# Performance work log

Measured on AMD Instinct MI355X. Metric: run time of the kernel, lower is better.

Reference implementation:

```python
import jax, jax.numpy as jnp
import numpy as np

DIM = 1024
H = 16
DH = DIM // H
NF = 64
EPS = 1e-6


def setup_inputs() -> dict:
    key = jax.random.key(0)
    ks = jax.random.split(key, 10)
    B, L = 4, 4096
    s = 1.0 / np.sqrt(DIM)
    x = jax.random.normal(ks[0], (B, L, DIM), dtype=jnp.float32)
    Wq = jax.random.normal(ks[1], (DIM, DIM), dtype=jnp.float32) * s
    Wk = jax.random.normal(ks[2], (DIM, DIM), dtype=jnp.float32) * s
    Wv = jax.random.normal(ks[3], (DIM, DIM), dtype=jnp.float32) * s
    Wo = jax.random.normal(ks[4], (DIM, DIM), dtype=jnp.float32) * s
    bq = jax.random.normal(ks[5], (DIM,), dtype=jnp.float32) * s
    bk = jax.random.normal(ks[6], (DIM,), dtype=jnp.float32) * s
    bv = jax.random.normal(ks[7], (DIM,), dtype=jnp.float32) * s
    bo = jax.random.normal(ks[8], (DIM,), dtype=jnp.float32) * s
    # random-feature buffer: [num_repeats=1, H, DH, NF]; use repeat 0
    Wrf = jax.random.normal(ks[9], (1, H, DH, NF), dtype=jnp.float32)
    return {"x": x, "Wq": Wq, "bq": bq, "Wk": Wk, "bk": bk, "Wv": Wv,
            "bv": bv, "Wo": Wo, "bo": bo, "Wrf": Wrf}


def reference(x, Wq, bq, Wk, bk, Wv, bv, Wo, bo, Wrf):
    B, L, _ = x.shape
    W0 = Wrf[0]  # [H, DH, NF]

    def split_heads(y):
        return y.reshape(B, L, H, DH).transpose(0, 2, 1, 3)  # [B,H,L,DH]

    q = split_heads(x @ Wq.T + bq)
    k = split_heads(x @ Wk.T + bk)
    v = split_heads(x @ Wv.T + bv)

    # key summary: logits [B,H,L,NF], softmax over flattened (L*NF)
    logits = jnp.einsum('bhld,hdf->bhlf', k, W0) \
             - 0.5 * jnp.sum(k * k, axis=-1, keepdims=True)
    alpha = jax.nn.softmax(logits.reshape(B, H, L * NF), axis=2)
    alpha = alpha.reshape(B, H, L, NF)
    N = jnp.einsum('bhlf,bhld->bhfd', alpha, v)  # [B,H,NF,DH]
    D = jnp.sum(alpha, axis=2)                   # [B,H,NF]

    # query feature map: per-position softmax over features
    phi = jax.nn.softmax(jnp.einsum('bhld,hdf->bhlf', q, W0), axis=-1)

    num = jnp.einsum('bhlf,bhfd->bhld', phi, N)
    den = jnp.einsum('bhlf,bhf->bhl', phi, D)
    out = num / (den[..., None] + EPS)

    ctx = out.transpose(0, 2, 1, 3).reshape(B, L, DIM)
    return ctx @ Wo.T + bo
```

## Files before the change

kernel.cpp:

```cpp
#include <hip/hip_runtime.h>
#include <hip/hip_bf16.h>

constexpr int NB   = 4;
constexpr int SL   = 4096;
constexpr int DIMC = 1024;
constexpr int NH   = 16;
constexpr int DHC  = 64;
constexpr int NFC  = 64;
constexpr int NCHK = 8;
constexpr float FEPS = 1e-6f;

typedef __attribute__((ext_vector_type(8))) short bf16x8_t;
typedef __attribute__((ext_vector_type(4))) float f32x4_t;
typedef __attribute__((ext_vector_type(4))) short s16x4_t;

__device__ __forceinline__ void load_lds_16B(const short* g, short* l) {
  __builtin_amdgcn_global_load_lds(
      (__attribute__((address_space(1))) void*)(g),
      (__attribute__((address_space(3))) void*)(l), 16, 0, 0);
}

__global__ __launch_bounds__(256) void cast_f32_to_bf16(
    const float* __restrict__ in, short* __restrict__ out, int n)
{
  const int i = (blockIdx.x * 256 + threadIdx.x) * 4;
  if (i >= n) return;
  const f32x4_t v = *(const f32x4_t*)(in + i);
  s16x4_t o;
#pragma unroll
  for (int j = 0; j < 4; j++) {
    __hip_bfloat16 h = __float2bfloat16(v[j]);
    o[j] = *(short*)&h;
  }
  *(s16x4_t*)(out + i) = o;
}

__global__ __launch_bounds__(256) void prep_w0t_kernel(
    const float* __restrict__ Wrf, short* __restrict__ Whi, short* __restrict__ Wlo)
{
  const int h = blockIdx.x;
  for (int t = threadIdx.x; t < 4096; t += 256) {
    const int f = t >> 6, dh = t & 63;
    const float w = Wrf[(size_t)h * 4096 + dh * 64 + f];
    __hip_bfloat16 hi = __float2bfloat16(w);
    const float rem = w - __bfloat162float(hi);
    __hip_bfloat16 lo = __float2bfloat16(rem);
    Whi[(size_t)h * 4096 + t] = *(short*)&hi;
    Wlo[(size_t)h * 4096 + t] = *(short*)&lo;
  }
}

__global__ __launch_bounds__(256) void fuse_w0_kernel(
    const float* __restrict__ Wq, const float* __restrict__ bq,
    const float* __restrict__ Wrf,
    short* __restrict__ Wfh, short* __restrict__ Wfl, float* __restrict__ bqf)
{
  const int h = blockIdx.x, cb = blockIdx.y;
  __shared__ float sWq[64][64];
  __shared__ float sW0[64][64];
  for (int idx = threadIdx.x; idx < 4096; idx += 256) {
    const int d = idx >> 6, e = idx & 63;
    sWq[d][e] = Wq[(size_t)(h * 64 + d) * 1024 + cb * 64 + e];
    sW0[d][e] = Wrf[(size_t)h * 4096 + d * 64 + e];
  }
  __syncthreads();
  for (int idx = threadIdx.x; idx < 4096; idx += 256) {
    const int f = idx >> 6, cc = idx & 63;
    float acc = 0.f;
#pragma unroll
    for (int d = 0; d < 64; d++) acc = fmaf(sWq[d][cc], sW0[d][f], acc);
    const __hip_bfloat16 hi = __float2bfloat16(acc);
    const float rem = acc - __bfloat162float(hi);
    const __hip_bfloat16 lo = __float2bfloat16(rem);
    Wfh[(size_t)(h * 64 + f) * 1024 + cb * 64 + cc] = *(const short*)&hi;
    Wfl[(size_t)(h * 64 + f) * 1024 + cb * 64 + cc] = *(const short*)&lo;
  }
  if (cb == 0 && threadIdx.x < 64) {
    const int f = threadIdx.x;
    float acc = 0.f;
#pragma unroll
    for (int d = 0; d < 64; d++) acc = fmaf(bq[h * 64 + d], sW0[d][f], acc);
    bqf[h * 64 + f] = acc;
  }
}

template <int MODE>
__global__ __launch_bounds__(256) void gemm_lds_kernel(
    const short* __restrict__ A, const short* __restrict__ W,
    const float* __restrict__ bias, void* __restrict__ C0,
    void* __restrict__ C1, float* __restrict__ Ks)
{
  constexpr int K = 1024, N = 1024;
  const int lane = threadIdx.x & 63;
  const int wid  = threadIdx.x >> 6;
  const int sub  = lane & 15;
  const int quad = lane >> 4;
  const int wr   = (wid >> 1) * 64;
  const int wc   = (wid & 1) * 64;
  const int row0 = blockIdx.x * 128;
  const int col0 = blockIdx.y * 128;

  __shared__ short As[128 * 64];
  __shared__ short Bs[128 * 64];

  f32x4_t acc[4][4] = {};

  const int srow = lane >> 3;
  for (int k0 = 0; k0 < K; k0 += 64) {
#pragma unroll
    for (int t = 0; t < 4; t++) {
      const int R   = wid * 32 + t * 8;
      const int row = R + srow;
      const int c   = (lane & 7) ^ (row & 7);
      load_lds_16B(A + (size_t)(row0 + row) * K + k0 + c * 8, As + R * 64);
      load_lds_16B(W + (size_t)(col0 + row) * K + k0 + c * 8, Bs + R * 64);
    }
    __syncthreads();

    bf16x8_t a[2][4], b[2][4];
#pragma unroll
    for (int ks = 0; ks < 2; ks++) {
#pragma unroll
      for (int i = 0; i < 4; i++) {
        const int ra = wr + i * 16 + sub;
        a[ks][i] = *(const bf16x8_t*)(As + ra * 64 + (((ks * 4 + quad) ^ (ra & 7)) * 8));
        const int rb = wc + i * 16 + sub;
        b[ks][i] = *(const bf16x8_t*)(Bs + rb * 64 + (((ks * 4 + quad) ^ (rb & 7)) * 8));
      }
    }
#pragma unroll
    for (int ks = 0; ks < 2; ks++)
#pragma unroll
      for (int i = 0; i < 4; i++)
#pragma unroll
        for (int j = 0; j < 4; j++) {
          if constexpr (MODE == 5)
            acc[i][j] = __builtin_amdgcn_mfma_f32_16x16x32_bf16(b[ks][j], a[ks][i], acc[i][j], 0, 0, 0);
          else
            acc[i][j] = __builtin_amdgcn_mfma_f32_16x16x32_bf16(a[ks][i], b[ks][j], acc[i][j], 0, 0, 0);
        }
    __syncthreads();
  }

  const int rb0 = row0 + wr;
  const int cb0 = col0 + wc;
  if constexpr (MODE == 3) {
    __hip_bfloat16* chi = (__hip_bfloat16*)C0;
    __hip_bfloat16* clo = (__hip_bfloat16*)C1;
    float s[4][4];
#pragma unroll
    for (int i = 0; i < 4; i++)
#pragma unroll
      for (int r = 0; r < 4; r++) s[i][r] = 0.f;
#pragma unroll
    for (int j = 0; j < 4; j++) {
      const int col = cb0 + j * 16 + sub;
      const float bv = bias[col];
#pragma unroll
      for (int i = 0; i < 4; i++) {
        const int row = rb0 + i * 16 + quad * 4;
#pragma unroll
        for (int r = 0; r < 4; r++) {
          const float val = acc[i][j][r] + bv;
          const __hip_bfloat16 hi = __float2bfloat16(val);
          const float rem = val - __bfloat162float(hi);
          chi[(size_t)(row + r) * N + col] = hi;
          clo[(size_t)(row + r) * N + col] = __float2bfloat16(rem);
          s[i][r] = fmaf(val, val, s[i][r]);
        }
      }
    }
    {
      const int head = cb0 >> 6;
#pragma unroll
      for (int o = 1; o < 16; o <<= 1)
#pragma unroll
        for (int i = 0; i < 4; i++)
#pragma unroll
          for (int r = 0; r < 4; r++) s[i][r] += __shfl_xor(s[i][r], o);
      if (sub == 0) {
#pragma unroll
        for (int i = 0; i < 4; i++)
#pragma unroll
          for (int r = 0; r < 4; r++)
            Ks[(size_t)(rb0 + i * 16 + quad * 4 + r) * NH + head] = s[i][r];
      }
    }
  } else if constexpr (MODE == 5) {
    __hip_bfloat16* vT = (__hip_bfloat16*)C0;
    const int bb    = row0 >> 12;
    const int lbase = rb0 - (bb << 12);
#pragma unroll
    for (int j = 0; j < 4; j++) {
#pragma unroll
      for (int r = 0; r < 4; r++) {
        const int col = cb0 + j * 16 + quad * 4 + r;
        const int h = col >> 6, d = col & 63;
        const float bv = bias[col];
        const size_t rowbase = ((size_t)((bb * NH + h) * 64 + d)) * (size_t)SL;
#pragma unroll
        for (int i = 0; i < 4; i++) {
          const int l = lbase + i * 16 + sub;
          const int pos = (l & ~127) | (((((l >> 3) & 15) ^ (d & 15)) << 3) | (l & 7));
          vT[rowbase + pos] = __float2bfloat16(acc[i][j][r] + bv);
        }
      }
    }
  } else {
#pragma unroll
    for (int j = 0; j < 4; j++) {
      const int col = cb0 + j * 16 + sub;
      const float bv = bias[col];
#pragma unroll
      for (int i = 0; i < 4; i++) {
        const int row = rb0 + i * 16 + quad * 4;
#pragma unroll
        for (int r = 0; r < 4; r++) {
          const float val = acc[i][j][r] + bv;
          ((float*)C0)[(size_t)(row + r) * N + col] = val;
        }
      }
    }
  }
}

__global__ __launch_bounds__(256) void gemm_phi_kernel(
    const short* __restrict__ A, const short* __restrict__ Wh,
    const short* __restrict__ Wl, const float* __restrict__ bqf,
    const float* __restrict__ Df, short* __restrict__ ehi,
    short* __restrict__ elo, float* __restrict__ sbuf)
{
  constexpr int K = 1024;
  const int lane = threadIdx.x & 63;
  const int wid  = threadIdx.x >> 6;
  const int sub  = lane & 15;
  const int quad = lane >> 4;
  const int wr   = (wid >> 1) * 64;
  const int wc   = (wid & 1) * 64;
  const int row0 = blockIdx.x * 128;
  const int col0 = blockIdx.y * 128;

  __shared__ short As[128 * 64];
  __shared__ short Bhs[128 * 64];
  __shared__ short Bls[128 * 64];

  f32x4_t acc[4][4] = {};

  const int srow = lane >> 3;
  for (int k0 = 0; k0 < K; k0 += 64) {
#pragma unroll
    for (int t = 0; t < 4; t++) {
      const int R   = wid * 32 + t * 8;
      const int row = R + srow;
      const int c   = (lane & 7) ^ (row & 7);
      load_lds_16B(A  + (size_t)(row0 + row) * K + k0 + c * 8, As  + R * 64);
      load_lds_16B(Wh + (size_t)(col0 + row) * K + k0 + c * 8, Bhs + R * 64);
      load_lds_16B(Wl + (size_t)(col0 + row) * K + k0 + c * 8, Bls + R * 64);
    }
    __syncthreads();

#pragma unroll
    for (int ks = 0; ks < 2; ks++) {
      bf16x8_t a[4], bh[4], bl[4];
#pragma unroll
      for (int i = 0; i < 4; i++) {
        const int ra = wr + i * 16 + sub;
        a[i] = *(const bf16x8_t*)(As + ra * 64 + (((ks * 4 + quad) ^ (ra & 7)) * 8));
        const int rb = wc + i * 16 + sub;
        bh[i] = *(const bf16x8_t*)(Bhs + rb * 64 + (((ks * 4 + quad) ^ (rb & 7)) * 8));
        bl[i] = *(const bf16x8_t*)(Bls + rb * 64 + (((ks * 4 + quad) ^ (rb & 7)) * 8));
      }
#pragma unroll
      for (int i = 0; i < 4; i++)
#pragma unroll
        for (int j = 0; j < 4; j++) {
          acc[i][j] = __builtin_amdgcn_mfma_f32_16x16x32_bf16(a[i], bh[j], acc[i][j], 0, 0, 0);
          acc[i][j] = __builtin_amdgcn_mfma_f32_16x16x32_bf16(a[i], bl[j], acc[i][j], 0, 0, 0);
        }
      __syncthreads();
    }
  }

  const int rb0 = row0 + wr;
  const int cb0 = col0 + wc;
  const int b   = row0 >> 12;
  const int h   = cb0 >> 6;
  float bv[4], Dl[4];
#pragma unroll
  for (int j = 0; j < 4; j++) {
    const int f = j * 16 + sub;
    bv[j] = bqf[h * 64 + f];
    Dl[j] = Df[(b * NH + h) * 64 + f];
  }
#pragma unroll
  for (int i = 0; i < 4; i++) {
#pragma unroll
    for (int r = 0; r < 4; r++) {
      float v[4];
#pragma unroll
      for (int j = 0; j < 4; j++) v[j] = acc[i][j][r] + bv[j];
      float mx = fmaxf(fmaxf(v[0], v[1]), fmaxf(v[2], v[3]));
#pragma unroll
      for (int o = 1; o < 16; o <<= 1) mx = fmaxf(mx, __shfl_xor(mx, o));
      float e[4], se = 0.f, dt = 0.f;
#pragma unroll
      for (int j = 0; j < 4; j++) {
        e[j] = __expf(v[j] - mx);
        se += e[j];
        dt = fmaf(e[j], Dl[j], dt);
      }
#pragma unroll
      for (int o = 1; o < 16; o <<= 1) { se += __shfl_xor(se, o); dt += __shfl_xor(dt, o); }

      const int row = rb0 + i * 16 + quad * 4 + r;
      const size_t base = (size_t)row * DIMC + h * 64;
#pragma unroll
      for (int j = 0; j < 4; j++) {
        const __hip_bfloat16 hi = __float2bfloat16(e[j]);
        const float rem = e[j] - __bfloat162float(hi);
        const __hip_bfloat16 lo = __float2bfloat16(rem);
        ehi[base + j * 16 + sub] = *(const short*)&hi;
        elo[base + j * 16 + sub] = *(const short*)&lo;
      }
      if (sub == 0) sbuf[row * NH + h] = 1.f / (dt + FEPS * se);
    }
  }
}

__global__ __launch_bounds__(256) void feat_gemm_kernel(
    const short* __restrict__ xhi, const short* __restrict__ xlo,
    const short* __restrict__ Whi, const short* __restrict__ Wlo,
    float* __restrict__ outlog)
{
  const int lane = threadIdx.x & 63, wid = threadIdx.x >> 6;
  const int sub = lane & 15, quad = lane >> 4;
  const int h = blockIdx.y;
  const int tok0 = blockIdx.x * 128 + wid * 32;
  const short* Bh = Whi + (size_t)h * 4096;
  const short* Bl = Wlo + (size_t)h * 4096;

  f32x4_t acc[2][4] = {};
#pragma unroll
  for (int ks = 0; ks < 2; ks++) {
    const int ko = ks * 32 + quad * 8;
    bf16x8_t ah[2], al[2], bh[4], bl[4];
#pragma unroll
    for (int i = 0; i < 2; i++) {
      const size_t base = (size_t)(tok0 + i * 16 + sub) * DIMC + h * 64 + ko;
      ah[i] = *(const bf16x8_t*)(xhi + base);
      al[i] = *(const bf16x8_t*)(xlo + base);
    }
#pragma unroll
    for (int j = 0; j < 4; j++) {
      const size_t base = (size_t)(j * 16 + sub) * 64 + ko;
      bh[j] = *(const bf16x8_t*)(Bh + base);
      bl[j] = *(const bf16x8_t*)(Bl + base);
    }
#pragma unroll
    for (int i = 0; i < 2; i++)
#pragma unroll
      for (int j = 0; j < 4; j++) {
        acc[i][j] = __builtin_amdgcn_mfma_f32_16x16x32_bf16(ah[i], bh[j], acc[i][j], 0, 0, 0);
        acc[i][j] = __builtin_amdgcn_mfma_f32_16x16x32_bf16(al[i], bh[j], acc[i][j], 0, 0, 0);
        acc[i][j] = __builtin_amdgcn_mfma_f32_16x16x32_bf16(ah[i], bl[j], acc[i][j], 0, 0, 0);
      }
  }
#pragma unroll
  for (int i = 0; i < 2; i++)
#pragma unroll
    for (int j = 0; j < 4; j++)
#pragma unroll
      for (int r = 0; r < 4; r++)
        outlog[(size_t)(tok0 + i * 16 + quad * 4 + r) * DIMC + h * 64 + j * 16 + sub] = acc[i][j][r];
}

__global__ __launch_bounds__(256) void kv_summary_mfma(
    const float* __restrict__ klog, const float* __restrict__ ksq,
    const short* __restrict__ vT, float* __restrict__ pN, float* __restrict__ pD)
{
  const int chunk = blockIdx.x, h = blockIdx.y, b = blockIdx.z;
  const int tid  = threadIdx.x;
  const int lane = tid & 63, wid = tid >> 6;
  const int sub  = lane & 15, quad = lane >> 4;

  __shared__ short vTs[64 * 128];
  __shared__ short wTh[64 * 128];
  __shared__ short wTl[64 * 128];

  f32x4_t accN[4] = {};
  f32x4_t accD = {};
  bf16x8_t bones;
#pragma unroll
  for (int e = 0; e < 8; e++) bones[e] = (sub == 0) ? (short)0x3F80 : (short)0;

  const int tw_t  = tid >> 1;
  const int tw_f0 = (tid & 1) * 32;

  const size_t vbase = ((size_t)((b * NH + h) * 64)) * (size_t)SL;
  const int fbase = (wid * 16 + sub) * 128;

  for (int it = 0; it < 4; ++it) {
    const int l0 = chunk * 512 + it * 128;

#pragma unroll
    for (int q = 0; q < 4; q++) {
      const int dbase = wid * 16 + q * 4;
      const int d = dbase + (lane >> 4);
      load_lds_16B(vT + vbase + (size_t)d * SL + l0 + (lane & 15) * 8,
                   vTs + dbase * 128);
    }

    {
      const int tok = b * SL + l0 + tw_t;
      const float kq = 0.5f * ksq[tok * NH + h];
      const float* kr = klog + (size_t)tok * DIMC + h * 64 + tw_f0;
      f32x4_t kl[8];
#pragma unroll
      for (int v4 = 0; v4 < 8; v4++) kl[v4] = *(const f32x4_t*)(kr + v4 * 4);
#pragma unroll
      for (int v4 = 0; v4 < 8; v4++) {
#pragma unroll
        for (int e = 0; e < 4; e++) {
          const int f = tw_f0 + v4 * 4 + e;
          const float wv = __expf(kl[v4][e] - kq);
          const __hip_bfloat16 hi = __float2bfloat16(wv);
          const float rem = wv - __bfloat162float(hi);
          const __hip_bfloat16 lo = __float2bfloat16(rem);
          const int p = f * 128 + (((((tw_t >> 3) & 15) ^ (f & 15)) << 3) | (tw_t & 7));
          wTh[p] = *(const short*)&hi;
          wTl[p] = *(const short*)&lo;
        }
      }
    }
    __syncthreads();

#pragma unroll
    for (int ks = 0; ks < 4; ks++) {
      const int ch = ks * 4 + quad;
      const bf16x8_t ah = *(const bf16x8_t*)(wTh + fbase + ((ch ^ sub) << 3));
      const bf16x8_t al = *(const bf16x8_t*)(wTl + fbase + ((ch ^ sub) << 3));
      accD = __builtin_amdgcn_mfma_f32_16x16x32_bf16(ah, bones, accD, 0, 0, 0);
      accD = __builtin_amdgcn_mfma_f32_16x16x32_bf16(al, bones, accD, 0, 0, 0);
#pragma unroll
      for (int j = 0; j < 4; j++) {
        const bf16x8_t bv = *(const bf16x8_t*)(vTs + (j * 16 + sub) * 128 + ((ch ^ sub) << 3));
        accN[j] = __builtin_amdgcn_mfma_f32_16x16x32_bf16(ah, bv, accN[j], 0, 0, 0);
        accN[j] = __builtin_amdgcn_mfma_f32_16x16x32_bf16(al, bv, accN[j], 0, 0, 0);
      }
    }
    __syncthreads();
  }

  const size_t pbase = (size_t)((b * NH + h) * NCHK + chunk);
#pragma unroll
  for (int j = 0; j < 4; j++)
#pragma unroll
    for (int r = 0; r < 4; r++)
      pN[pbase * 4096 + (wid * 16 + quad * 4 + r) * 64 + j * 16 + sub] = accN[j][r];
  if (sub == 0) {
#pragma unroll
    for (int r = 0; r < 4; r++)
      pD[pbase * 64 + wid * 16 + quad * 4 + r] = accD[r];
  }
}

__global__ __launch_bounds__(256) void combine_nd_kernel(
    const float* __restrict__ pN, const float* __restrict__ pD,
    short* __restrict__ NfTh, short* __restrict__ NfTl, float* __restrict__ Df)
{
  const int bh = blockIdx.x, seg = blockIdx.y;
  __shared__ float sInv;
  float dsum = 0.f;
  if (threadIdx.x < 64) {
    for (int c = 0; c < NCHK; c++)
      dsum += pD[(size_t)(bh * NCHK + c) * 64 + threadIdx.x];
    float s = dsum;
#pragma unroll
    for (int o = 32; o; o >>= 1) s += __shfl_xor(s, o);
    if (threadIdx.x == 0) sInv = 1.f / s;
  }
  __syncthreads();
  const float inv = sInv;
  if (seg == 0 && threadIdx.x < 64) Df[bh * 64 + threadIdx.x] = dsum * inv;
  const int t = seg * 256 + threadIdx.x;
  float acc = 0.f;
  for (int c = 0; c < NCHK; c++)
    acc += pN[((size_t)(bh * NCHK + c)) * 4096 + t];
  const float val = acc * inv;
  const int f = t >> 6, d = t & 63;
  const __hip_bfloat16 hi = __float2bfloat16(val);
  const float rem = val - __bfloat162float(hi);
  const __hip_bfloat16 lo = __float2bfloat16(rem);
  NfTh[(size_t)bh * 4096 + d * 64 + f] = *(const short*)&hi;
  NfTl[(size_t)bh * 4096 + d * 64 + f] = *(const short*)&lo;
}

__global__ __launch_bounds__(256) void ctx_gemm_kernel(
    const short* __restrict__ ehi, const short* __restrict__ elo,
    const short* __restrict__ NfTh, const short* __restrict__ NfTl,
    const float* __restrict__ sbuf, __hip_bfloat16* __restrict__ ctx)
{
  const int lane = threadIdx.x & 63, wid = threadIdx.x >> 6;
  const int sub = lane & 15, quad = lane >> 4;
  const int h = blockIdx.y;
  const int tok0 = blockIdx.x * 128 + wid * 32;
  const int b = blockIdx.x >> 5;
  const short* Bh = NfTh + ((size_t)(b * NH + h)) * 4096;
  const short* Bl = NfTl + ((size_t)(b * NH + h)) * 4096;

  f32x4_t acc[2][4] = {};
#pragma unroll
  for (int ks = 0; ks < 2; ks++) {
    const int ko = ks * 32 + quad * 8;
    bf16x8_t ah[2], al[2], bh[4], bl[4];
#pragma unroll
    for (int i = 0; i < 2; i++) {
      const size_t base = (size_t)(tok0 + i * 16 + sub) * DIMC + h * 64 + ko;
      ah[i] = *(const bf16x8_t*)(ehi + base);
      al[i] = *(const bf16x8_t*)(elo + base);
    }
#pragma unroll
    for (int j = 0; j < 4; j++) {
      const size_t base = (size_t)(j * 16 + sub) * 64 + ko;
      bh[j] = *(const bf16x8_t*)(Bh + base);
      bl[j] = *(const bf16x8_t*)(Bl + base);
    }
#pragma unroll
    for (int i = 0; i < 2; i++)
#pragma unroll
      for (int j = 0; j < 4; j++) {
        acc[i][j] = __builtin_amdgcn_mfma_f32_16x16x32_bf16(ah[i], bh[j], acc[i][j], 0, 0, 0);
        acc[i][j] = __builtin_amdgcn_mfma_f32_16x16x32_bf16(al[i], bh[j], acc[i][j], 0, 0, 0);
        acc[i][j] = __builtin_amdgcn_mfma_f32_16x16x32_bf16(ah[i], bl[j], acc[i][j], 0, 0, 0);
      }
  }
#pragma unroll
  for (int i = 0; i < 2; i++)
#pragma unroll
    for (int r = 0; r < 4; r++) {
      const int token = tok0 + i * 16 + quad * 4 + r;
      const float sv = sbuf[token * NH + h];
#pragma unroll
      for (int j = 0; j < 4; j++)
        ctx[(size_t)token * DIMC + h * 64 + j * 16 + sub] =
            __float2bfloat16(acc[i][j][r] * sv);
    }
}

extern "C" void kernel_launch(void* const* d_in, const int* in_sizes, int n_in,
                              void* d_out, int out_size, void* d_ws, size_t ws_size,
                              hipStream_t stream) {
  (void)in_sizes; (void)n_in; (void)out_size; (void)ws_size;
  const float* x   = (const float*)d_in[0];
  const float* Wq  = (const float*)d_in[1];
  const float* bq  = (const float*)d_in[2];
  const float* Wk  = (const float*)d_in[3];
  const float* bk  = (const float*)d_in[4];
  const float* Wv  = (const float*)d_in[5];
  const float* bv  = (const float*)d_in[6];
  const float* Wo  = (const float*)d_in[7];
  const float* bo  = (const float*)d_in[8];
  const float* Wrf = (const float*)d_in[9];
  float* out = (float*)d_out;

  constexpr size_t MiB = 1u << 20;
  constexpr size_t KiB = 1u << 10;
  constexpr size_t NTOK = (size_t)NB * SL;
  constexpr size_t XN   = NTOK * DIMC;
  constexpr size_t WN   = (size_t)DIMC * DIMC;

  char* ws = (char*)d_ws;
  short* xb   = (short*)(ws);
  short* Wkb  = (short*)(ws + 32 * MiB);
  short* Wvb  = (short*)(ws + 34 * MiB);
  short* Wob  = (short*)(ws + 36 * MiB);
  short* W0Th = (short*)(ws + 40 * MiB);
  short* W0Tl = (short*)(ws + 40 * MiB + 128 * KiB);
  float* bqf  = (float*)(ws + 40 * MiB + 256 * KiB);
  float* ksq  = (float*)(ws + 41 * MiB);
  float* sbuf = (float*)(ws + 42 * MiB);
  float* pD   = (float*)(ws + 43 * MiB);
  short* NfTh = (short*)(ws + 43 * MiB + 512 * KiB);
  short* NfTl = (short*)(ws + 44 * MiB);
  float* Df   = (float*)(ws + 44 * MiB + 512 * KiB);
  float* klog = (float*)(ws + 45 * MiB);
  __hip_bfloat16* khi = (__hip_bfloat16*)(ws + 109 * MiB);
  __hip_bfloat16* klo = (__hip_bfloat16*)(ws + 141 * MiB);
  short* vTb  = (short*)(ws + 173 * MiB);
  float* pN   = (float*)(ws + 109 * MiB);
  short* Wqfh = (short*)(ws + 173 * MiB);
  short* Wqfl = (short*)(ws + 175 * MiB);
  short* ehi  = (short*)(ws + 45 * MiB);
  short* elo  = (short*)(ws + 77 * MiB);
  __hip_bfloat16* ctxb = (__hip_bfloat16*)xb;

  const dim3 blk(256);

  cast_f32_to_bf16<<<dim3(XN / 1024), blk, 0, stream>>>(x, xb, (int)XN);
  cast_f32_to_bf16<<<dim3(WN / 1024), blk, 0, stream>>>(Wk, Wkb, (int)WN);
  cast_f32_to_bf16<<<dim3(WN / 1024), blk, 0, stream>>>(Wv, Wvb, (int)WN);
  cast_f32_to_bf16<<<dim3(WN / 1024), blk, 0, stream>>>(Wo, Wob, (int)WN);
  prep_w0t_kernel<<<dim3(NH), blk, 0, stream>>>(Wrf, W0Th, W0Tl);

  const dim3 gg(NTOK / 128, DIMC / 128);
  gemm_lds_kernel<3><<<gg, blk, 0, stream>>>(xb, Wkb, bk, khi, klo, ksq);
  gemm_lds_kernel<5><<<gg, blk, 0, stream>>>(xb, Wvb, bv, vTb, nullptr, nullptr);

  feat_gemm_kernel<<<dim3(NTOK / 128, NH), blk, 0, stream>>>(
      (const short*)khi, (const short*)klo, W0Th, W0Tl, klog);

  kv_summary_mfma<<<dim3(NCHK, NH, NB), blk, 0, stream>>>(klog, ksq, vTb, pN, pD);
  fuse_w0_kernel<<<dim3(NH, 16), blk, 0, stream>>>(Wq, bq, Wrf, Wqfh, Wqfl, bqf);
  combine_nd_kernel<<<dim3(NB * NH, 16), blk, 0, stream>>>(pN, pD, NfTh, NfTl, Df);

  gemm_phi_kernel<<<gg, blk, 0, stream>>>(xb, Wqfh, Wqfl, bqf, Df, ehi, elo, sbuf);
  ctx_gemm_kernel<<<dim3(NTOK / 128, NH), blk, 0, stream>>>(
      ehi, elo, NfTh, NfTl, sbuf, ctxb);

  gemm_lds_kernel<0><<<gg, blk, 0, stream>>>((const short*)ctxb, Wob, bo, out, nullptr, nullptr);
}
```

Baseline: 491.1 us.

## Fuse key feature GEMM into KV summary kernel, dropping fp32 logit buffer

The separate feat_gemm kernel that wrote fp32 key logits (64 MiB) to global memory is removed. The kv summary kernel now loads the hi/lo bf16 key tiles and W0 into LDS, computes the logits with MFMA in-block, applies the exp, and reuses the LDS buffers for the transposed weights. This removes a large global write and read plus one launch. The cost is the logit GEMM running inside a small grid of 512 blocks, with an extra barrier and more LDS per block.

```diff
diff --git a/kernel.cpp b/kernel.cpp
--- a/kernel.cpp
+++ b/kernel.cpp
@@ -327,56 +327,11 @@
   }
 }
 
-__global__ __launch_bounds__(256) void feat_gemm_kernel(
-    const short* __restrict__ xhi, const short* __restrict__ xlo,
-    const short* __restrict__ Whi, const short* __restrict__ Wlo,
-    float* __restrict__ outlog)
-{
-  const int lane = threadIdx.x & 63, wid = threadIdx.x >> 6;
-  const int sub = lane & 15, quad = lane >> 4;
-  const int h = blockIdx.y;
-  const int tok0 = blockIdx.x * 128 + wid * 32;
-  const short* Bh = Whi + (size_t)h * 4096;
-  const short* Bl = Wlo + (size_t)h * 4096;
-
-  f32x4_t acc[2][4] = {};
-#pragma unroll
-  for (int ks = 0; ks < 2; ks++) {
-    const int ko = ks * 32 + quad * 8;
-    bf16x8_t ah[2], al[2], bh[4], bl[4];
-#pragma unroll
-    for (int i = 0; i < 2; i++) {
-      const size_t base = (size_t)(tok0 + i * 16 + sub) * DIMC + h * 64 + ko;
-      ah[i] = *(const bf16x8_t*)(xhi + base);
-      al[i] = *(const bf16x8_t*)(xlo + base);
-    }
-#pragma unroll
-    for (int j = 0; j < 4; j++) {
-      const size_t base = (size_t)(j * 16 + sub) * 64 + ko;
-      bh[j] = *(const bf16x8_t*)(Bh + base);
-      bl[j] = *(const bf16x8_t*)(Bl + base);
-    }
-#pragma unroll
-    for (int i = 0; i < 2; i++)
-#pragma unroll
-      for (int j = 0; j < 4; j++) {
-        acc[i][j] = __builtin_amdgcn_mfma_f32_16x16x32_bf16(ah[i], bh[j], acc[i][j], 0, 0, 0);
-        acc[i][j] = __builtin_amdgcn_mfma_f32_16x16x32_bf16(al[i], bh[j], acc[i][j], 0, 0, 0);
-        acc[i][j] = __builtin_amdgcn_mfma_f32_16x16x32_bf16(ah[i], bl[j], acc[i][j], 0, 0, 0);
-      }
-  }
-#pragma unroll
-  for (int i = 0; i < 2; i++)
-#pragma unroll
-    for (int j = 0; j < 4; j++)
-#pragma unroll
-      for (int r = 0; r < 4; r++)
-        outlog[(size_t)(tok0 + i * 16 + quad * 4 + r) * DIMC + h * 64 + j * 16 + sub] = acc[i][j][r];
-}
-
-__global__ __launch_bounds__(256) void kv_summary_mfma(
-    const float* __restrict__ klog, const float* __restrict__ ksq,
-    const short* __restrict__ vT, float* __restrict__ pN, float* __restrict__ pD)
+__global__ __launch_bounds__(256) void kv_fused_kernel(
+    const short* __restrict__ khi, const short* __restrict__ klo,
+    const short* __restrict__ W0h, const short* __restrict__ W0l,
+    const float* __restrict__ ksq, const short* __restrict__ vT,
+    float* __restrict__ pN, float* __restrict__ pD)
 {
   const int chunk = blockIdx.x, h = blockIdx.y, b = blockIdx.z;
   const int tid  = threadIdx.x;
@@ -384,8 +339,10 @@
   const int sub  = lane & 15, quad = lane >> 4;
 
   __shared__ short vTs[64 * 128];
-  __shared__ short wTh[64 * 128];
-  __shared__ short wTl[64 * 128];
+  __shared__ short w0hs[64 * 64];
+  __shared__ short w0ls[64 * 64];
+  __shared__ short uh[128 * 64];
+  __shared__ short ul[128 * 64];
 
   f32x4_t accN[4] = {};
   f32x4_t accD = {};
@@ -393,8 +350,14 @@
 #pragma unroll
   for (int e = 0; e < 8; e++) bones[e] = (sub == 0) ? (short)0x3F80 : (short)0;
 
-  const int tw_t  = tid >> 1;
-  const int tw_f0 = (tid & 1) * 32;
+#pragma unroll
+  for (int t = 0; t < 2; t++) {
+    const int R   = wid * 16 + t * 8;
+    const int row = R + (lane >> 3);
+    const int c   = (lane & 7) ^ (row & 7);
+    load_lds_16B(W0h + (size_t)h * 4096 + row * 64 + c * 8, w0hs + R * 64);
+    load_lds_16B(W0l + (size_t)h * 4096 + row * 64 + c * 8, w0ls + R * 64);
+  }
 
   const size_t vbase = ((size_t)((b * NH + h) * 64)) * (size_t)SL;
   const int fbase = (wid * 16 + sub) * 128;
@@ -409,26 +372,62 @@
       load_lds_16B(vT + vbase + (size_t)d * SL + l0 + (lane & 15) * 8,
                    vTs + dbase * 128);
     }
-
-    {
-      const int tok = b * SL + l0 + tw_t;
-      const float kq = 0.5f * ksq[tok * NH + h];
-      const float* kr = klog + (size_t)tok * DIMC + h * 64 + tw_f0;
-      f32x4_t kl[8];
-#pragma unroll
-      for (int v4 = 0; v4 < 8; v4++) kl[v4] = *(const f32x4_t*)(kr + v4 * 4);
-#pragma unroll
-      for (int v4 = 0; v4 < 8; v4++) {
-#pragma unroll
-        for (int e = 0; e < 4; e++) {
-          const int f = tw_f0 + v4 * 4 + e;
-          const float wv = __expf(kl[v4][e] - kq);
+#pragma unroll
+    for (int t = 0; t < 4; t++) {
+      const int R   = wid * 32 + t * 8;
+      const int row = R + (lane >> 3);
+      const int c   = (lane & 7) ^ (row & 7);
+      const size_t src = (size_t)(b * SL + l0 + row) * DIMC + h * 64 + c * 8;
+      load_lds_16B(khi + src, uh + R * 64);
+      load_lds_16B(klo + src, ul + R * 64);
+    }
+    __syncthreads();
+
+    f32x4_t kacc[2][4] = {};
+#pragma unroll
+    for (int ks = 0; ks < 2; ks++) {
+      bf16x8_t ah[2], al[2], b0[4], b1[4];
+#pragma unroll
+      for (int i = 0; i < 2; i++) {
+        const int ra  = wid * 32 + i * 16 + sub;
+        const int off = ra * 64 + (((ks * 4 + quad) ^ (ra & 7)) * 8);
+        ah[i] = *(const bf16x8_t*)(uh + off);
+        al[i] = *(const bf16x8_t*)(ul + off);
+      }
+#pragma unroll
+      for (int j = 0; j < 4; j++) {
+        const int rb  = j * 16 + sub;
+        const int off = rb * 64 + (((ks * 4 + quad) ^ (rb & 7)) * 8);
+        b0[j] = *(const bf16x8_t*)(w0hs + off);
+        b1[j] = *(const bf16x8_t*)(w0ls + off);
+      }
+#pragma unroll
+      for (int i = 0; i < 2; i++)
+#pragma unroll
+        for (int j = 0; j < 4; j++) {
+          kacc[i][j] = __builtin_amdgcn_mfma_f32_16x16x32_bf16(ah[i], b0[j], kacc[i][j], 0, 0, 0);
+          kacc[i][j] = __builtin_amdgcn_mfma_f32_16x16x32_bf16(al[i], b0[j], kacc[i][j], 0, 0, 0);
+          kacc[i][j] = __builtin_amdgcn_mfma_f32_16x16x32_bf16(ah[i], b1[j], kacc[i][j], 0, 0, 0);
+        }
+    }
+    __syncthreads();
+
+#pragma unroll
+    for (int i = 0; i < 2; i++) {
+#pragma unroll
+      for (int r = 0; r < 4; r++) {
+        const int tok = wid * 32 + i * 16 + quad * 4 + r;
+        const float kq = 0.5f * ksq[(size_t)(b * SL + l0 + tok) * NH + h];
+#pragma unroll
+        for (int j = 0; j < 4; j++) {
+          const int f = j * 16 + sub;
+          const float wv = __expf(kacc[i][j][r] - kq);
           const __hip_bfloat16 hi = __float2bfloat16(wv);
           const float rem = wv - __bfloat162float(hi);
           const __hip_bfloat16 lo = __float2bfloat16(rem);
-          const int p = f * 128 + (((((tw_t >> 3) & 15) ^ (f & 15)) << 3) | (tw_t & 7));
-          wTh[p] = *(const short*)&hi;
-          wTl[p] = *(const short*)&lo;
+          const int p = f * 128 + (((((tok >> 3) & 15) ^ (f & 15)) << 3) | (tok & 7));
+          uh[p] = *(const short*)&hi;
+          ul[p] = *(const short*)&lo;
         }
       }
     }
@@ -437,8 +436,8 @@
 #pragma unroll
     for (int ks = 0; ks < 4; ks++) {
       const int ch = ks * 4 + quad;
-      const bf16x8_t ah = *(const bf16x8_t*)(wTh + fbase + ((ch ^ sub) << 3));
-      const bf16x8_t al = *(const bf16x8_t*)(wTl + fbase + ((ch ^ sub) << 3));
+      const bf16x8_t ah = *(const bf16x8_t*)(uh + fbase + ((ch ^ sub) << 3));
+      const bf16x8_t al = *(const bf16x8_t*)(ul + fbase + ((ch ^ sub) << 3));
       accD = __builtin_amdgcn_mfma_f32_16x16x32_bf16(ah, bones, accD, 0, 0, 0);
       accD = __builtin_amdgcn_mfma_f32_16x16x32_bf16(al, bones, accD, 0, 0, 0);
 #pragma unroll
@@ -583,11 +582,10 @@
   short* NfTh = (short*)(ws + 43 * MiB + 512 * KiB);
   short* NfTl = (short*)(ws + 44 * MiB);
   float* Df   = (float*)(ws + 44 * MiB + 512 * KiB);
-  float* klog = (float*)(ws + 45 * MiB);
+  float* pN   = (float*)(ws + 45 * MiB);
   __hip_bfloat16* khi = (__hip_bfloat16*)(ws + 109 * MiB);
   __hip_bfloat16* klo = (__hip_bfloat16*)(ws + 141 * MiB);
   short* vTb  = (short*)(ws + 173 * MiB);
-  float* pN   = (float*)(ws + 109 * MiB);
   short* Wqfh = (short*)(ws + 173 * MiB);
   short* Wqfl = (short*)(ws + 175 * MiB);
   short* ehi  = (short*)(ws + 45 * MiB);
@@ -606,10 +604,8 @@
   gemm_lds_kernel<3><<<gg, blk, 0, stream>>>(xb, Wkb, bk, khi, klo, ksq);
   gemm_lds_kernel<5><<<gg, blk, 0, stream>>>(xb, Wvb, bv, vTb, nullptr, nullptr);
 
-  feat_gemm_kernel<<<dim3(NTOK / 128, NH), blk, 0, stream>>>(
-      (const short*)khi, (const short*)klo, W0Th, W0Tl, klog);
-
-  kv_summary_mfma<<<dim3(NCHK, NH, NB), blk, 0, stream>>>(klog, ksq, vTb, pN, pD);
+  kv_fused_kernel<<<dim3(NCHK, NH, NB), blk, 0, stream>>>(
+      (const short*)khi, (const short*)klo, W0Th, W0Tl, ksq, vTb, pN, pD);
   fuse_w0_kernel<<<dim3(NH, 16), blk, 0, stream>>>(Wq, bq, Wrf, Wqfh, Wqfl, bqf);
   combine_nd_kernel<<<dim3(NB * NH, 16), blk, 0, stream>>>(pN, pD, NfTh, NfTl, Df);
 
```

After: 459.5 us. 1.07x faster.
